# Performance work log

Hardware: AMD Instinct MI355X
Metric: run time of the kernel (lower is better)

The kernel has to match this reference:

```python
import jax, jax.numpy as jnp
import numpy as np

B, S, H = 64, 512, 768
N_SPANS, MAX_SPAN, CW = 4, 8, 3
NH = 8
HD = H // NH
W = MAX_SPAN + 1 + 2 * CW  # max context window length (15)
H2 = H // 2
N_ATE, N_SENT = 2, 2


def _ln(x, g, b, eps=1e-5):
    m = x.mean(-1, keepdims=True)
    v = ((x - m) ** 2).mean(-1, keepdims=True)
    return (x - m) / jnp.sqrt(v + eps) * g + b


def _classifier(x, w1, b1, g, bb, w2, b2):
    # Dropout -> Linear -> GELU -> LayerNorm -> Linear (eval mode: dropout = id)
    h = jax.nn.gelu(x @ w1.T + b1, approximate=False)
    h = _ln(h, g, bb)
    return h @ w2.T + b2


def setup_inputs() -> dict:
    key = jax.random.key(0)
    ks = jax.random.split(key, 16)
    p = lambda k, shape: (0.02 * jax.random.normal(k, shape)).astype(jnp.float32)
    seq_out = jax.random.normal(ks[0], (B, S, H), dtype=jnp.float32)
    starts = jax.random.randint(ks[1], (B, N_SPANS), 1, S - MAX_SPAN - 1)
    lens = jax.random.randint(ks[2], (B, N_SPANS), 1, MAX_SPAN + 1)
    ends = starts + lens  # exclusive end, span length in [1, MAX_SPAN]
    return dict(
        seq_out=seq_out,
        span_starts=starts.astype(jnp.int32),
        span_ends=ends.astype(jnp.int32),
        ate_g=jnp.ones((H,), jnp.float32), ate_b=jnp.zeros((H,), jnp.float32),
        apc_g=jnp.ones((H,), jnp.float32), apc_b=jnp.zeros((H,), jnp.float32),
        w_in=p(ks[3], (3 * H, H)), b_in=jnp.zeros((3 * H,), jnp.float32),
        w_out=p(ks[4], (H, H)), b_out=jnp.zeros((H,), jnp.float32),
        fus_w=p(ks[5], (H, 2 * H)), fus_b=jnp.zeros((H,), jnp.float32),
        asp_w1=p(ks[6], (H2, H)), asp_b1=jnp.zeros((H2,), jnp.float32),
        asp_lng=jnp.ones((H2,), jnp.float32), asp_lnb=jnp.zeros((H2,), jnp.float32),
        asp_w2=p(ks[7], (N_ATE, H2)), asp_b2=jnp.zeros((N_ATE,), jnp.float32),
        sen_w1=p(ks[8], (H2, H)), sen_b1=jnp.zeros((H2,), jnp.float32),
        sen_lng=jnp.ones((H2,), jnp.float32), sen_lnb=jnp.zeros((H2,), jnp.float32),
        sen_w2=p(ks[9], (N_SENT, H2)), sen_b2=jnp.zeros((N_SENT,), jnp.float32),
    )


def _fwd(seq_out, ate_g, ate_b, apc_g, apc_b, w_in, b_in, w_out, b_out,
         fus_w, fus_b, asp_w1, asp_b1, asp_lng, asp_lnb, asp_w2, asp_b2,
         sen_w1, sen_b1, sen_lng, sen_lnb, sen_w2, sen_b2,
         span_starts, span_ends):
    dt = seq_out.dtype
    # clamping semantics as in the torch loop
    s = jnp.clip(span_starts, 0, S - 1)
    e = jnp.maximum(s, jnp.minimum(span_ends, S - 1))
    left = jnp.maximum(0, s - CW)
    right = jnp.minimum(S, e + 1 + CW)

    # ATE head over all tokens
    ate_logits = _classifier(_ln(seq_out, ate_g, ate_b),
                             asp_w1, asp_b1, asp_lng, asp_lnb, asp_w2, asp_b2)

    gather = jax.vmap(lambda so, idx: so[idx])  # ([S,H],[N,W]) -> [N,W,H]

    # aspect mean over tokens [s, e)
    aidx = s[..., None] + jnp.arange(MAX_SPAN)          # [B,N,MS]
    va = (aidx < e[..., None]).astype(dt)
    asp_tok = gather(seq_out, jnp.clip(aidx, 0, S - 1)) # [B,N,MS,H]
    cnt = va.sum(-1, keepdims=True)                     # [B,N,1]
    asp_mean = (asp_tok * va[..., None]).sum(-2) / jnp.maximum(cnt, 1.0)
    asp_mean = jnp.where(cnt > 0, asp_mean, seq_out[:, None, 0, :])

    # context window [left, right): tiny self-attention, then mean
    cidx = left[..., None] + jnp.arange(W)              # [B,N,W]
    vc = (cidx < right[..., None]).astype(dt)
    ctx = gather(seq_out, jnp.clip(cidx, 0, S - 1))     # [B,N,W,H]
    qkv = ctx @ w_in.T + b_in
    q, k, v = jnp.split(qkv, 3, axis=-1)
    q = q.reshape(B, N_SPANS, W, NH, HD) * (HD ** -0.5)
    k = k.reshape(B, N_SPANS, W, NH, HD)
    v = v.reshape(B, N_SPANS, W, NH, HD)
    scores = jnp.einsum('bnqhd,bnkhd->bnhqk', q, k)
    neg = jnp.asarray(jnp.finfo(dt).min, dt)
    scores = jnp.where(vc[:, :, None, None, :] > 0, scores, neg)
    attn = jax.nn.softmax(scores, axis=-1)
    out = jnp.einsum('bnhqk,bnkhd->bnqhd', attn, v).reshape(B, N_SPANS, W, H)
    out = out @ w_out.T + b_out
    ccnt = vc.sum(-1, keepdims=True)
    ctx_mean = (out * vc[..., None]).sum(-2) / jnp.maximum(ccnt, 1.0)

    combined = jnp.concatenate([asp_mean, ctx_mean], axis=-1)  # [B,N,2H]
    fused = jax.nn.gelu(combined @ fus_w.T + fus_b, approximate=False)
    apc_feat = fused.mean(axis=1)                              # [B,H]
    apc_logits = _classifier(_ln(apc_feat, apc_g, apc_b),
                             sen_w1, sen_b1, sen_lng, sen_lnb, sen_w2, sen_b2)
    return ate_logits, apc_logits


def reference(seq_out, span_starts, span_ends, ate_g, ate_b, apc_g, apc_b,
              w_in, b_in, w_out, b_out, fus_w, fus_b,
              asp_w1, asp_b1, asp_lng, asp_lnb, asp_w2, asp_b2,
              sen_w1, sen_b1, sen_lng, sen_lnb, sen_w2, sen_b2):
    return _fwd(seq_out, ate_g, ate_b, apc_g, apc_b, w_in, b_in, w_out, b_out,
                fus_w, fus_b, asp_w1, asp_b1, asp_lng, asp_lnb, asp_w2, asp_b2,
                sen_w1, sen_b1, sen_lng, sen_lnb, sen_w2, sen_b2,
                span_starts, span_ends)
```

## Files before the change

### kernel.cpp

```cpp
#include <hip/hip_runtime.h>
#include <math.h>

#define DEVI __device__ __forceinline__

using bf16x8 = __attribute__((ext_vector_type(8))) short;
using f32x4  = __attribute__((ext_vector_type(4))) float;

DEVI float b2f(unsigned short u) {
  union { unsigned int u; float f; } x; x.u = ((unsigned int)u) << 16; return x.f;
}
DEVI unsigned short f2b(float f) {
  union { float f; unsigned int u; } x; x.f = f;
  unsigned int r = (x.u + 0x7fffu + ((x.u >> 16) & 1u)) >> 16;
  return (unsigned short)r;
}
DEVI float gelu_f(float x) { return 0.5f * x * (1.0f + erff(x * 0.70710678118654752440f)); }

DEVI void wredxor2(float& a, float& b) {
  #pragma unroll
  for (int off = 32; off; off >>= 1) {
    a += __shfl_xor(a, off);
    b += __shfl_xor(b, off);
  }
}

template<int NW>
DEVI void breduce2(float& a, float& b) {
  __shared__ float buf[2 * NW];
  int lane = threadIdx.x & 63;
  int w = threadIdx.x >> 6;
  #pragma unroll
  for (int off = 32; off > 0; off >>= 1) {
    a += __shfl_down(a, off);
    b += __shfl_down(b, off);
  }
  if (lane == 0) { buf[w] = a; buf[NW + w] = b; }
  __syncthreads();
  float ra = 0.f, rb = 0.f;
  #pragma unroll
  for (int i = 0; i < NW; ++i) { ra += buf[i]; rb += buf[NW + i]; }
  a = ra; b = rb;
  __syncthreads();
}

DEVI void span_params(const int* st, const int* en, int span,
                      int& s, int& e, int& left, int& right) {
  int s0 = st[span], e0 = en[span];
  s = min(max(s0, 0), 511);
  e = max(s, min(e0, 511));
  left = max(0, s - 3);
  right = min(512, e + 4);
}

DEVI int xcd_logical(int bid, int n) {
  int q = n >> 3, r = n & 7;
  int xcd = bid & 7, idx = bid >> 3;
  return (xcd < r ? xcd * (q + 1) : r * (q + 1) + (xcd - r) * q) + idx;
}

__global__ __launch_bounds__(256) void prep_kernel(
    const float* __restrict__ s0, const float* __restrict__ s1,
    const float* __restrict__ s2, const float* __restrict__ s3,
    const float* __restrict__ s4,
    unsigned short* __restrict__ d0, unsigned short* __restrict__ d1,
    unsigned short* __restrict__ d2, unsigned short* __restrict__ d3,
    unsigned short* __restrict__ d4,
    const float* __restrict__ seq, const float* __restrict__ ate_g,
    const float* __restrict__ ate_b, unsigned short* __restrict__ lnx,
    const int* __restrict__ st, const int* __restrict__ en,
    unsigned short* __restrict__ ctxA) {
  const int bid = blockIdx.x, tid = threadIdx.x;
  if (bid < 4032) {
    int i = bid * 256 + tid;
    const float* s; unsigned short* d; int j;
    if (i < 73728)       { s = s0; d = d0; j = i; }
    else if (i < 516096) { s = s1; d = d1; j = i - 73728; }
    else if (i < 663552) { s = s2; d = d2; j = i - 516096; }
    else if (i < 958464) { s = s3; d = d3; j = i - 663552; }
    else                 { s = s4; d = d4; j = i - 958464; }
    float4 v = reinterpret_cast<const float4*>(s)[j];
    ushort4 o;
    o.x = f2b(v.x); o.y = f2b(v.y); o.z = f2b(v.z); o.w = f2b(v.w);
    reinterpret_cast<ushort4*>(d)[j] = o;
  } else if (bid < 12224) {
    const int row = (bid - 4032) * 4 + (tid >> 6);
    const int lane = tid & 63;
    const float4* xr = reinterpret_cast<const float4*>(seq + (size_t)row * 768);
    float4 v[3];
    #pragma unroll
    for (int j = 0; j < 3; ++j) v[j] = xr[j * 64 + lane];
    float s = 0.f, q = 0.f;
    #pragma unroll
    for (int j = 0; j < 3; ++j) {
      s += v[j].x + v[j].y + v[j].z + v[j].w;
      q += v[j].x * v[j].x + v[j].y * v[j].y + v[j].z * v[j].z + v[j].w * v[j].w;
    }
    wredxor2(s, q);
    float mean = s * (1.0f / 768.0f);
    float rstd = rsqrtf(q * (1.0f / 768.0f) - mean * mean + 1e-5f);
    ushort4* orow = reinterpret_cast<ushort4*>(lnx + (size_t)row * 768);
    #pragma unroll
    for (int j = 0; j < 3; ++j) {
      float4 gv = reinterpret_cast<const float4*>(ate_g)[j * 64 + lane];
      float4 bv = reinterpret_cast<const float4*>(ate_b)[j * 64 + lane];
      ushort4 o;
      o.x = f2b((v[j].x - mean) * rstd * gv.x + bv.x);
      o.y = f2b((v[j].y - mean) * rstd * gv.y + bv.y);
      o.z = f2b((v[j].z - mean) * rstd * gv.z + bv.z);
      o.w = f2b((v[j].w - mean) * rstd * gv.w + bv.w);
      orow[j * 64 + lane] = o;
    }
  } else {
    if (tid >= 192) return;
    int r = bid - 12224;
    int span = r / 15, w = r % 15;
    int s, e, left, right;
    span_params(st, en, span, s, e, left, right);
    int b = span >> 2;
    int tok = min(left + w, 511);
    const float4* src = reinterpret_cast<const float4*>(seq + ((size_t)b * 512 + tok) * 768);
    ushort4* dst = reinterpret_cast<ushort4*>(ctxA + (size_t)r * 768);
    float4 v = src[tid];
    ushort4 o;
    o.x = f2b(v.x); o.y = f2b(v.y); o.z = f2b(v.z); o.w = f2b(v.w);
    dst[tid] = o;
  }
}

template<int BM, int BN, int WM, int WN>
DEVI void gemm_core(const unsigned short* __restrict__ A,
                    const unsigned short* __restrict__ W,
                    int K, int bm, int bn,
                    unsigned short* As, unsigned short* Bs,
                    f32x4 (&acc)[WM / 16][WN / 16]) {
  constexpr int CA = BM / 8;
  constexpr int CB = BN / 8;
  constexpr int NWC = BN / WN;
  constexpr int WAVES = (BM / WM) * NWC;
  constexpr int FM = WM / 16, FN = WN / 16;
  const int tid = threadIdx.x;
  const int lane = tid & 63;
  const int wv = tid >> 6;
  const int wr = wv / NWC, wc = wv % NWC;
  const int l16 = lane & 15, lhi = lane >> 4;
  const int srow = lane >> 3;
  const int scol = 8 * ((lane & 7) ^ srow);

  const int nt = K / 64;
  for (int t = 0; t < nt; ++t) {
    const int k0 = t * 64;
    #pragma unroll
    for (int ch = wv; ch < CA; ch += WAVES)
      __builtin_amdgcn_global_load_lds(
          (const __attribute__((address_space(1))) void*)&A[(size_t)(bm + ch * 8 + srow) * K + k0 + scol],
          (__attribute__((address_space(3))) void*)&As[ch * 512], 16, 0, 0);
    #pragma unroll
    for (int ch = wv; ch < CB; ch += WAVES)
      __builtin_amdgcn_global_load_lds(
          (const __attribute__((address_space(1))) void*)&W[(size_t)(bn + ch * 8 + srow) * K + k0 + scol],
          (__attribute__((address_space(3))) void*)&Bs[ch * 512], 16, 0, 0);
    __syncthreads();
    #pragma unroll
    for (int kk = 0; kk < 2; ++kk) {
      bf16x8 af[FM], bfr[FN];
      #pragma unroll
      for (int fm = 0; fm < FM; ++fm) {
        int r = wr * WM + fm * 16 + l16;
        af[fm] = *reinterpret_cast<const bf16x8*>(&As[r * 64 + ((kk * 32 + lhi * 8) ^ ((r & 7) * 8))]);
      }
      #pragma unroll
      for (int fn = 0; fn < FN; ++fn) {
        int r = wc * WN + fn * 16 + l16;
        bfr[fn] = *reinterpret_cast<const bf16x8*>(&Bs[r * 64 + ((kk * 32 + lhi * 8) ^ ((r & 7) * 8))]);
      }
      #pragma unroll
      for (int fm = 0; fm < FM; ++fm)
        #pragma unroll
        for (int fn = 0; fn < FN; ++fn)
          acc[fm][fn] = __builtin_amdgcn_mfma_f32_16x16x32_bf16(af[fm], bfr[fn], acc[fm][fn], 0, 0, 0);
    }
    __syncthreads();
  }
}

template<int BM, int BN, int WM, int WN>
DEVI void gemm_store(const float* __restrict__ bias, unsigned short* __restrict__ C,
                     int N, bool act, int bm, int bn, f32x4 (&acc)[WM / 16][WN / 16]) {
  constexpr int NWC = BN / WN;
  constexpr int FM = WM / 16, FN = WN / 16;
  const int lane = threadIdx.x & 63;
  const int wv = threadIdx.x >> 6;
  const int wr = wv / NWC, wc = wv % NWC;
  const int l16 = lane & 15, lhi = lane >> 4;
  #pragma unroll
  for (int fm = 0; fm < FM; ++fm) {
    #pragma unroll
    for (int fn = 0; fn < FN; ++fn) {
      int col = bn + wc * WN + fn * 16 + l16;
      float bv = bias[col];
      #pragma unroll
      for (int i = 0; i < 4; ++i) {
        int row = bm + wr * WM + fm * 16 + lhi * 4 + i;
        float v = acc[fm][fn][i] + bv;
        if (act) v = gelu_f(v);
        C[(size_t)row * N + col] = f2b(v);
      }
    }
  }
}

template<int BM, int BN, int WM, int WN, int ACT>
__global__ __launch_bounds__(256) void gemm_swz64(
    const unsigned short* __restrict__ A, const unsigned short* __restrict__ W,
    const float* __restrict__ bias, unsigned short* __restrict__ C,
    int M, int N, int K, int nbN) {
  __shared__ __align__(16) unsigned short As[BM * 64];
  __shared__ __align__(16) unsigned short Bs[BN * 64];
  int l = xcd_logical(blockIdx.x, gridDim.x);
  int mb = l / nbN, nb = l % nbN;
  f32x4 acc[WM / 16][WN / 16] = {};
  gemm_core<BM, BN, WM, WN>(A, W, K, mb * BM, nb * BN, As, Bs, acc);
  gemm_store<BM, BN, WM, WN>(bias, C, N, ACT != 0, mb * BM, nb * BN, acc);
}

__global__ __launch_bounds__(512) void dual_gemm_kernel(
    const unsigned short* __restrict__ lnx, const unsigned short* __restrict__ w1b,
    const float* __restrict__ b1, const float* __restrict__ lng,
    const float* __restrict__ w2, float4* __restrict__ hpart,
    const unsigned short* __restrict__ ctxA, const unsigned short* __restrict__ winb,
    const float* __restrict__ b_in, unsigned short* __restrict__ qkv) {
  __shared__ __align__(16) unsigned short lds[384 * 64];
  if (blockIdx.x < 384) {
    int l = xcd_logical(blockIdx.x, 384);
    int mb = l / 3, nb = l % 3;
    const int bm = mb * 256, bn = nb * 128;
    f32x4 acc[4][4] = {};
    gemm_core<256, 128, 64, 64>(lnx, w1b, 768, bm, bn, lds, lds + 256 * 64, acc);
    const int lane = threadIdx.x & 63;
    const int wv = threadIdx.x >> 6;
    const int wr = wv >> 1, wc = wv & 1;
    const int l16 = lane & 15, lhi = lane >> 4;
    float b1v[4], gw2a[4], gw2b[4];
    #pragma unroll
    for (int fn = 0; fn < 4; ++fn) {
      int col = bn + wc * 64 + fn * 16 + l16;
      b1v[fn] = b1[col];
      float gg = lng[col];
      gw2a[fn] = gg * w2[col];
      gw2b[fn] = gg * w2[384 + col];
    }
    #pragma unroll
    for (int fm = 0; fm < 4; ++fm) {
      #pragma unroll
      for (int i = 0; i < 4; ++i) {
        float s1 = 0.f, s2 = 0.f, q0 = 0.f, q1 = 0.f;
        #pragma unroll
        for (int fn = 0; fn < 4; ++fn) {
          float h = gelu_f(acc[fm][fn][i] + b1v[fn]);
          s1 += h; s2 += h * h;
          q0 += h * gw2a[fn]; q1 += h * gw2b[fn];
        }
        #pragma unroll
        for (int off = 1; off < 16; off <<= 1) {
          s1 += __shfl_xor(s1, off); s2 += __shfl_xor(s2, off);
          q0 += __shfl_xor(q0, off); q1 += __shfl_xor(q1, off);
        }
        if (l16 == 0) {
          int row = bm + wr * 64 + fm * 16 + lhi * 4 + i;
          hpart[(size_t)row * 6 + nb * 2 + wc] = make_float4(s1, s2, q0, q1);
        }
      }
    }
  } else {
    int bid = blockIdx.x - 384;
    int l = xcd_logical(bid, 270);
    int mb = l / 9, nb = l % 9;
    f32x4 acc[4][4] = {};
    gemm_core<128, 256, 64, 64>(ctxA, winb, 768, mb * 128, nb * 256,
                                lds, lds + 128 * 64, acc);
    gemm_store<128, 256, 64, 64>(b_in, qkv, 2304, false, mb * 128, nb * 256, acc);
  }
}

__global__ __launch_bounds__(256) void finattn_kernel(
    const float4* __restrict__ hpart, const float* __restrict__ lng,
    const float* __restrict__ lnb, const float* __restrict__ w2,
    const float* __restrict__ b2, float* __restrict__ out,
    const unsigned short* __restrict__ qkv, const int* __restrict__ st,
    const int* __restrict__ en, unsigned short* __restrict__ ctxO) {
  const int tid = threadIdx.x;
  if (blockIdx.x >= 2048) {
    __shared__ float cbuf[16];
    float c1a = 0.f, c1b = 0.f, c2a = 0.f, c2b = 0.f;
    for (int c = tid; c < 384; c += 256) {
      float gg = lng[c], bbv = lnb[c], wa = w2[c], wb = w2[384 + c];
      c1a += gg * wa; c1b += gg * wb;
      c2a += bbv * wa; c2b += bbv * wb;
    }
    wredxor2(c1a, c1b);
    wredxor2(c2a, c2b);
    if ((tid & 63) == 0) {
      int w = tid >> 6;
      cbuf[w * 4] = c1a; cbuf[w * 4 + 1] = c1b;
      cbuf[w * 4 + 2] = c2a; cbuf[w * 4 + 3] = c2b;
    }
    __syncthreads();
    c1a = cbuf[0] + cbuf[4] + cbuf[8] + cbuf[12];
    c1b = cbuf[1] + cbuf[5] + cbuf[9] + cbuf[13];
    c2a = cbuf[2] + cbuf[6] + cbuf[10] + cbuf[14];
    c2b = cbuf[3] + cbuf[7] + cbuf[11] + cbuf[15];
    const int row = (blockIdx.x - 2048) * 256 + tid;
    float S1 = 0.f, S2 = 0.f, D0 = 0.f, D1 = 0.f;
    #pragma unroll
    for (int p = 0; p < 6; ++p) {
      float4 v = hpart[(size_t)row * 6 + p];
      S1 += v.x; S2 += v.y; D0 += v.z; D1 += v.w;
    }
    float mu = S1 * (1.f / 384.f);
    float rstd = rsqrtf(S2 * (1.f / 384.f) - mu * mu + 1e-5f);
    out[(size_t)row * 2]     = rstd * (D0 - mu * c1a) + c2a + b2[0];
    out[(size_t)row * 2 + 1] = rstd * (D1 - mu * c1b) + c2b + b2[1];
    return;
  }
  __shared__ float qs[15][96], ks[15][96], vs[15][96];
  __shared__ float sc[15][16];
  const int span = blockIdx.x >> 3, hh = blockIdx.x & 7;
  int s, e, left, right;
  span_params(st, en, span, s, e, left, right);
  const int nv = right - left;
  const int r0 = span * 15;
  const float scale = 0.10206207261596576f;
  if (tid < 180) {
    int w = tid / 12, dp = tid % 12, d = dp * 8;
    const unsigned short* rowp = qkv + (size_t)(r0 + w) * 2304 + hh * 96 + d;
    bf16x8 qv = *reinterpret_cast<const bf16x8*>(rowp);
    bf16x8 kv = *reinterpret_cast<const bf16x8*>(rowp + 768);
    bf16x8 vv = *reinterpret_cast<const bf16x8*>(rowp + 1536);
    #pragma unroll
    for (int j = 0; j < 8; ++j) {
      qs[w][d + j] = b2f((unsigned short)qv[j]) * scale;
      ks[w][d + j] = b2f((unsigned short)kv[j]);
      vs[w][d + j] = b2f((unsigned short)vv[j]);
    }
  }
  __syncthreads();
  if (tid < 225) {
    int i = tid / 15, j = tid % 15;
    float a = 0.f;
    #pragma unroll
    for (int d = 0; d < 96; ++d) a += qs[i][d] * ks[j][d];
    sc[i][j] = (j < nv) ? a : -3.402823466e38f;
  }
  __syncthreads();
  if (tid < 15) {
    int i = tid;
    float m = -3.402823466e38f;
    #pragma unroll
    for (int j = 0; j < 15; ++j) m = fmaxf(m, sc[i][j]);
    float ex[15];
    float ssum = 0.f;
    #pragma unroll
    for (int j = 0; j < 15; ++j) { ex[j] = expf(sc[i][j] - m); ssum += ex[j]; }
    float inv = 1.0f / ssum;
    #pragma unroll
    for (int j = 0; j < 15; ++j) sc[i][j] = ex[j] * inv;
  }
  __syncthreads();
  for (int idx = tid; idx < 720; idx += 256) {
    int w = idx / 48, dp = idx % 48, d = dp * 2;
    float o0 = 0.f, o1 = 0.f;
    #pragma unroll
    for (int j = 0; j < 15; ++j) {
      float p = sc[w][j];
      o0 += p * vs[j][d];
      o1 += p * vs[j][d + 1];
    }
    ushort2 o; o.x = f2b(o0); o.y = f2b(o1);
    *reinterpret_cast<ushort2*>(&ctxO[(size_t)(r0 + w) * 768 + hh * 96 + d]) = o;
  }
}

__global__ __launch_bounds__(256) void means_kernel(
    const float* __restrict__ seq, const unsigned short* __restrict__ projO,
    const int* __restrict__ st, const int* __restrict__ en,
    unsigned short* __restrict__ comb) {
  const int span = blockIdx.x;
  int s, e, left, right;
  span_params(st, en, span, s, e, left, right);
  int b = span >> 2;
  int e2 = min(e, s + 8);
  int cnt = e2 - s;
  int nv = right - left;
  float inva = (cnt > 0) ? 1.0f / (float)cnt : 0.f;
  float invc = 1.0f / (float)nv;
  for (int c = threadIdx.x; c < 768; c += 256) {
    float sa = 0.f;
    for (int t = s; t < e2; ++t) sa += seq[((size_t)b * 512 + t) * 768 + c];
    float asp = (cnt > 0) ? sa * inva : seq[((size_t)b * 512) * 768 + c];
    comb[(size_t)span * 1536 + c] = f2b(asp);
    float sc_ = 0.f;
    for (int w = 0; w < nv; ++w) sc_ += b2f(projO[(size_t)(span * 15 + w) * 768 + c]);
    comb[(size_t)span * 1536 + 768 + c] = f2b(sc_ * invc);
  }
}

__global__ __launch_bounds__(256) void apc_all_kernel(
    const unsigned short* __restrict__ fused, const float* __restrict__ g,
    const float* __restrict__ bb, const unsigned short* __restrict__ senb,
    const float* __restrict__ b1, const float* __restrict__ lng,
    const float* __restrict__ lnb, const float* __restrict__ w2,
    const float* __restrict__ b2, float* __restrict__ out) {
  const int b = blockIdx.x, tid = threadIdx.x;
  __shared__ float xs[768];
  __shared__ float hs[384];
  float v[3];
  #pragma unroll
  for (int j = 0; j < 3; ++j) {
    int c = tid + j * 256;
    float a = 0.f;
    #pragma unroll
    for (int n = 0; n < 4; ++n) a += b2f(fused[((size_t)(b * 4 + n)) * 768 + c]);
    v[j] = 0.25f * a;
  }
  float s = v[0] + v[1] + v[2];
  float q = v[0] * v[0] + v[1] * v[1] + v[2] * v[2];
  breduce2<4>(s, q);
  float mean = s * (1.f / 768.f);
  float rstd = rsqrtf(q * (1.f / 768.f) - mean * mean + 1e-5f);
  #pragma unroll
  for (int j = 0; j < 3; ++j) {
    int c = tid + j * 256;
    xs[c] = (v[j] - mean) * rstd * g[c] + bb[c];
  }
  __syncthreads();
  for (int j = tid; j < 384; j += 256) {
    const bf16x8* wrp = reinterpret_cast<const bf16x8*>(senb + (size_t)j * 768);
    float dot = 0.f;
    #pragma unroll 4
    for (int k8 = 0; k8 < 96; ++k8) {
      bf16x8 wv = wrp[k8];
      #pragma unroll
      for (int u = 0; u < 8; ++u) dot += xs[k8 * 8 + u] * b2f((unsigned short)wv[u]);
    }
    hs[j] = gelu_f(dot + b1[j]);
  }
  __syncthreads();
  s = 0.f; q = 0.f;
  for (int j = tid; j < 384; j += 256) { float h = hs[j]; s += h; q += h * h; }
  breduce2<4>(s, q);
  mean = s * (1.f / 384.f);
  rstd = rsqrtf(q * (1.f / 384.f) - mean * mean + 1e-5f);
  float p0 = 0.f, p1 = 0.f;
  for (int j = tid; j < 384; j += 256) {
    float hl = (hs[j] - mean) * rstd * lng[j] + lnb[j];
    p0 += hl * w2[j];
    p1 += hl * w2[384 + j];
  }
  breduce2<4>(p0, p1);
  if (tid == 0) {
    out[b * 2]     = p0 + b2[0];
    out[b * 2 + 1] = p1 + b2[1];
  }
}

extern "C" void kernel_launch(void* const* d_in, const int* in_sizes, int n_in,
                              void* d_out, int out_size, void* d_ws, size_t ws_size,
                              hipStream_t stream) {
  const float* seq    = (const float*)d_in[0];
  const int*   st     = (const int*)d_in[1];
  const int*   en     = (const int*)d_in[2];
  const float* ate_g  = (const float*)d_in[3];
  const float* ate_b  = (const float*)d_in[4];
  const float* apc_g  = (const float*)d_in[5];
  const float* apc_b  = (const float*)d_in[6];
  const float* w_in   = (const float*)d_in[7];
  const float* b_in   = (const float*)d_in[8];
  const float* w_out  = (const float*)d_in[9];
  const float* b_out  = (const float*)d_in[10];
  const float* fus_w  = (const float*)d_in[11];
  const float* fus_b  = (const float*)d_in[12];
  const float* asp_w1 = (const float*)d_in[13];
  const float* asp_b1 = (const float*)d_in[14];
  const float* asp_lng= (const float*)d_in[15];
  const float* asp_lnb= (const float*)d_in[16];
  const float* asp_w2 = (const float*)d_in[17];
  const float* asp_b2 = (const float*)d_in[18];
  const float* sen_w1 = (const float*)d_in[19];
  const float* sen_b1 = (const float*)d_in[20];
  const float* sen_lng= (const float*)d_in[21];
  const float* sen_lnb= (const float*)d_in[22];
  const float* sen_w2 = (const float*)d_in[23];
  const float* sen_b2 = (const float*)d_in[24];
  float* out = (float*)d_out;

  char* wsb = (char*)d_ws;
  unsigned short* lnx   = (unsigned short*)(wsb + 0);
  unsigned short* ctxA  = (unsigned short*)(wsb + 52428800);
  unsigned short* qkvb  = (unsigned short*)(wsb + 58720256);
  unsigned short* ctxO  = (unsigned short*)(wsb + 77594624);
  unsigned short* projO = (unsigned short*)(wsb + 83886080);
  unsigned short* comb  = (unsigned short*)(wsb + 89849856);
  unsigned short* fusO  = (unsigned short*)(wsb + 90636288);
  const size_t off_w = 91275264;
  float4*        hpart  = (float4*)(wsb + off_w);
  const size_t off_w2 = off_w + 25165824;
  unsigned short* w1b   = (unsigned short*)(wsb + off_w2);
  unsigned short* winb  = (unsigned short*)(wsb + off_w2 + 589824);
  unsigned short* woutb = (unsigned short*)(wsb + off_w2 + 4128768);
  unsigned short* fusb  = (unsigned short*)(wsb + off_w2 + 5308416);
  unsigned short* senb  = (unsigned short*)(wsb + off_w2 + 7667712);

  prep_kernel<<<16064, 256, 0, stream>>>(asp_w1, w_in, w_out, fus_w, sen_w1,
                                         w1b, winb, woutb, fusb, senb,
                                         seq, ate_g, ate_b, lnx, st, en, ctxA);
  dual_gemm_kernel<<<654, 512, 0, stream>>>(lnx, w1b, asp_b1, asp_lng, asp_w2, hpart,
                                            ctxA, winb, b_in, qkvb);
  finattn_kernel<<<2176, 256, 0, stream>>>(hpart, asp_lng, asp_lnb, asp_w2, asp_b2, out,
                                           qkvb, st, en, ctxO);
  gemm_swz64<64, 128, 32, 64, 0><<<360, 256, 0, stream>>>(
      ctxO, woutb, b_out, projO, 3840, 768, 768, 6);
  means_kernel<<<256, 256, 0, stream>>>(seq, projO, st, en, comb);
  gemm_swz64<64, 64, 32, 32, 1><<<48, 256, 0, stream>>>(
      comb, fusb, fus_b, fusO, 256, 768, 1536, 12);
  apc_all_kernel<<<64, 256, 0, stream>>>(fusO, apc_g, apc_b, senb, sen_b1,
                                         sen_lng, sen_lnb, sen_w2, sen_b2, out + 65536);
}
```

Before: 183.2 us.

## Fold LayerNorm into ATE GEMM epilogue and gather context rows via token map

The ATE LayerNorm is now applied algebraically. The gamma scale is folded into the bf16 W1 weights, and per-row (rstd, rstd*mean) stats plus per-column gamma·W and beta·W sums correct the raw-input GEMM in the epilogue. As a result one bf16 copy of seq serves the ATE GEMM, the QKV GEMM (through a row index map instead of a materialized context copy) and the means kernel, which now reads bf16 instead of fp32. This cuts the separate normalized-activation and context buffers and the related traffic. In exchange it adds a tiny serial dot-product pass for the correction sums, and the algebraic LN in bf16 carries some precision risk.

```diff
diff --git a/kernel.cpp b/kernel.cpp
--- a/kernel.cpp
+++ b/kernel.cpp
@@ -59,25 +59,35 @@
 }
 
 __global__ __launch_bounds__(256) void prep_kernel(
-    const float* __restrict__ s0, const float* __restrict__ s1,
-    const float* __restrict__ s2, const float* __restrict__ s3,
-    const float* __restrict__ s4,
+    const float* __restrict__ w1, const float* __restrict__ w_in,
+    const float* __restrict__ w_out, const float* __restrict__ fus_w,
+    const float* __restrict__ sen_w1,
     unsigned short* __restrict__ d0, unsigned short* __restrict__ d1,
     unsigned short* __restrict__ d2, unsigned short* __restrict__ d3,
     unsigned short* __restrict__ d4,
     const float* __restrict__ seq, const float* __restrict__ ate_g,
-    const float* __restrict__ ate_b, unsigned short* __restrict__ lnx,
+    const float* __restrict__ ate_b, unsigned short* __restrict__ sbf,
+    float2* __restrict__ stats, float2* __restrict__ c12,
     const int* __restrict__ st, const int* __restrict__ en,
-    unsigned short* __restrict__ ctxA) {
+    int* __restrict__ tokmap) {
   const int bid = blockIdx.x, tid = threadIdx.x;
   if (bid < 4032) {
     int i = bid * 256 + tid;
+    if (i < 73728) {
+      float4 v = reinterpret_cast<const float4*>(w1)[i];
+      int k0 = (i * 4) % 768;
+      float4 gv = *reinterpret_cast<const float4*>(ate_g + k0);
+      ushort4 o;
+      o.x = f2b(v.x * gv.x); o.y = f2b(v.y * gv.y);
+      o.z = f2b(v.z * gv.z); o.w = f2b(v.w * gv.w);
+      reinterpret_cast<ushort4*>(d0)[i] = o;
+      return;
+    }
     const float* s; unsigned short* d; int j;
-    if (i < 73728)       { s = s0; d = d0; j = i; }
-    else if (i < 516096) { s = s1; d = d1; j = i - 73728; }
-    else if (i < 663552) { s = s2; d = d2; j = i - 516096; }
-    else if (i < 958464) { s = s3; d = d3; j = i - 663552; }
-    else                 { s = s4; d = d4; j = i - 958464; }
+    if (i < 516096)      { s = w_in;   d = d1; j = i - 73728; }
+    else if (i < 663552) { s = w_out;  d = d2; j = i - 516096; }
+    else if (i < 958464) { s = fus_w;  d = d3; j = i - 663552; }
+    else                 { s = sen_w1; d = d4; j = i - 958464; }
     float4 v = reinterpret_cast<const float4*>(s)[j];
     ushort4 o;
     o.x = f2b(v.x); o.y = f2b(v.y); o.z = f2b(v.z); o.w = f2b(v.w);
@@ -98,32 +108,34 @@
     wredxor2(s, q);
     float mean = s * (1.0f / 768.0f);
     float rstd = rsqrtf(q * (1.0f / 768.0f) - mean * mean + 1e-5f);
-    ushort4* orow = reinterpret_cast<ushort4*>(lnx + (size_t)row * 768);
+    ushort4* orow = reinterpret_cast<ushort4*>(sbf + (size_t)row * 768);
     #pragma unroll
     for (int j = 0; j < 3; ++j) {
-      float4 gv = reinterpret_cast<const float4*>(ate_g)[j * 64 + lane];
-      float4 bv = reinterpret_cast<const float4*>(ate_b)[j * 64 + lane];
       ushort4 o;
-      o.x = f2b((v[j].x - mean) * rstd * gv.x + bv.x);
-      o.y = f2b((v[j].y - mean) * rstd * gv.y + bv.y);
-      o.z = f2b((v[j].z - mean) * rstd * gv.z + bv.z);
-      o.w = f2b((v[j].w - mean) * rstd * gv.w + bv.w);
+      o.x = f2b(v[j].x); o.y = f2b(v[j].y); o.z = f2b(v[j].z); o.w = f2b(v[j].w);
       orow[j * 64 + lane] = o;
     }
+    if (lane == 0) stats[row] = make_float2(rstd, rstd * mean);
+  } else if (bid < 12226) {
+    int j = (bid - 12224) * 256 + tid;
+    if (j < 384) {
+      const float* wr = w1 + (size_t)j * 768;
+      float a = 0.f, bsum = 0.f;
+      for (int k = 0; k < 768; ++k) {
+        float wv = wr[k];
+        a += ate_g[k] * wv;
+        bsum += ate_b[k] * wv;
+      }
+      c12[j] = make_float2(a, bsum);
+    }
   } else {
-    if (tid >= 192) return;
-    int r = bid - 12224;
-    int span = r / 15, w = r % 15;
-    int s, e, left, right;
-    span_params(st, en, span, s, e, left, right);
-    int b = span >> 2;
-    int tok = min(left + w, 511);
-    const float4* src = reinterpret_cast<const float4*>(seq + ((size_t)b * 512 + tok) * 768);
-    ushort4* dst = reinterpret_cast<ushort4*>(ctxA + (size_t)r * 768);
-    float4 v = src[tid];
-    ushort4 o;
-    o.x = f2b(v.x); o.y = f2b(v.y); o.z = f2b(v.z); o.w = f2b(v.w);
-    dst[tid] = o;
+    for (int i = tid; i < 3840; i += 256) {
+      int span = i / 15, w = i % 15;
+      int s, e, left, right;
+      span_params(st, en, span, s, e, left, right);
+      int b = span >> 2;
+      tokmap[i] = b * 512 + min(left + w, 511);
+    }
   }
 }
 
@@ -132,7 +144,8 @@
                     const unsigned short* __restrict__ W,
                     int K, int bm, int bn,
                     unsigned short* As, unsigned short* Bs,
-                    f32x4 (&acc)[WM / 16][WN / 16]) {
+                    f32x4 (&acc)[WM / 16][WN / 16],
+                    const int* __restrict__ rowmap = nullptr) {
   constexpr int CA = BM / 8;
   constexpr int CB = BN / 8;
   constexpr int NWC = BN / WN;
@@ -150,10 +163,13 @@
   for (int t = 0; t < nt; ++t) {
     const int k0 = t * 64;
     #pragma unroll
-    for (int ch = wv; ch < CA; ch += WAVES)
+    for (int ch = wv; ch < CA; ch += WAVES) {
+      int ar = bm + ch * 8 + srow;
+      size_t arow = rowmap ? (size_t)rowmap[ar] : (size_t)ar;
       __builtin_amdgcn_global_load_lds(
-          (const __attribute__((address_space(1))) void*)&A[(size_t)(bm + ch * 8 + srow) * K + k0 + scol],
+          (const __attribute__((address_space(1))) void*)&A[arow * K + k0 + scol],
           (__attribute__((address_space(3))) void*)&As[ch * 512], 16, 0, 0);
+    }
     #pragma unroll
     for (int ch = wv; ch < CB; ch += WAVES)
       __builtin_amdgcn_global_load_lds(
@@ -224,27 +240,30 @@
 }
 
 __global__ __launch_bounds__(512) void dual_gemm_kernel(
-    const unsigned short* __restrict__ lnx, const unsigned short* __restrict__ w1b,
-    const float* __restrict__ b1, const float* __restrict__ lng,
+    const unsigned short* __restrict__ sbf, const unsigned short* __restrict__ w1b,
+    const float* __restrict__ b1, const float2* __restrict__ c12,
+    const float2* __restrict__ stats, const float* __restrict__ lng,
     const float* __restrict__ w2, float4* __restrict__ hpart,
-    const unsigned short* __restrict__ ctxA, const unsigned short* __restrict__ winb,
-    const float* __restrict__ b_in, unsigned short* __restrict__ qkv) {
+    const unsigned short* __restrict__ winb, const float* __restrict__ b_in,
+    unsigned short* __restrict__ qkv, const int* __restrict__ tokmap) {
   __shared__ __align__(16) unsigned short lds[384 * 64];
   if (blockIdx.x < 384) {
     int l = xcd_logical(blockIdx.x, 384);
     int mb = l / 3, nb = l % 3;
     const int bm = mb * 256, bn = nb * 128;
     f32x4 acc[4][4] = {};
-    gemm_core<256, 128, 64, 64>(lnx, w1b, 768, bm, bn, lds, lds + 256 * 64, acc);
+    gemm_core<256, 128, 64, 64>(sbf, w1b, 768, bm, bn, lds, lds + 256 * 64, acc);
     const int lane = threadIdx.x & 63;
     const int wv = threadIdx.x >> 6;
     const int wr = wv >> 1, wc = wv & 1;
     const int l16 = lane & 15, lhi = lane >> 4;
-    float b1v[4], gw2a[4], gw2b[4];
+    float b1v[4], gw2a[4], gw2b[4], c1v[4], c2v[4];
     #pragma unroll
     for (int fn = 0; fn < 4; ++fn) {
       int col = bn + wc * 64 + fn * 16 + l16;
       b1v[fn] = b1[col];
+      float2 cc = c12[col];
+      c1v[fn] = cc.x; c2v[fn] = cc.y;
       float gg = lng[col];
       gw2a[fn] = gg * w2[col];
       gw2b[fn] = gg * w2[384 + col];
@@ -253,10 +272,12 @@
     for (int fm = 0; fm < 4; ++fm) {
       #pragma unroll
       for (int i = 0; i < 4; ++i) {
+        int row = bm + wr * 64 + fm * 16 + lhi * 4 + i;
+        float2 sr = stats[row];
         float s1 = 0.f, s2 = 0.f, q0 = 0.f, q1 = 0.f;
         #pragma unroll
         for (int fn = 0; fn < 4; ++fn) {
-          float h = gelu_f(acc[fm][fn][i] + b1v[fn]);
+          float h = gelu_f(sr.x * acc[fm][fn][i] - sr.y * c1v[fn] + c2v[fn] + b1v[fn]);
           s1 += h; s2 += h * h;
           q0 += h * gw2a[fn]; q1 += h * gw2b[fn];
         }
@@ -265,10 +286,7 @@
           s1 += __shfl_xor(s1, off); s2 += __shfl_xor(s2, off);
           q0 += __shfl_xor(q0, off); q1 += __shfl_xor(q1, off);
         }
-        if (l16 == 0) {
-          int row = bm + wr * 64 + fm * 16 + lhi * 4 + i;
-          hpart[(size_t)row * 6 + nb * 2 + wc] = make_float4(s1, s2, q0, q1);
-        }
+        if (l16 == 0) hpart[(size_t)row * 6 + nb * 2 + wc] = make_float4(s1, s2, q0, q1);
       }
     }
   } else {
@@ -276,8 +294,8 @@
     int l = xcd_logical(bid, 270);
     int mb = l / 9, nb = l % 9;
     f32x4 acc[4][4] = {};
-    gemm_core<128, 256, 64, 64>(ctxA, winb, 768, mb * 128, nb * 256,
-                                lds, lds + 128 * 64, acc);
+    gemm_core<128, 256, 64, 64>(sbf, winb, 768, mb * 128, nb * 256,
+                                lds, lds + 128 * 64, acc, tokmap);
     gemm_store<128, 256, 64, 64>(b_in, qkv, 2304, false, mb * 128, nb * 256, acc);
   }
 }
@@ -381,7 +399,7 @@
 }
 
 __global__ __launch_bounds__(256) void means_kernel(
-    const float* __restrict__ seq, const unsigned short* __restrict__ projO,
+    const unsigned short* __restrict__ sbf, const unsigned short* __restrict__ projO,
     const int* __restrict__ st, const int* __restrict__ en,
     unsigned short* __restrict__ comb) {
   const int span = blockIdx.x;
@@ -395,8 +413,8 @@
   float invc = 1.0f / (float)nv;
   for (int c = threadIdx.x; c < 768; c += 256) {
     float sa = 0.f;
-    for (int t = s; t < e2; ++t) sa += seq[((size_t)b * 512 + t) * 768 + c];
-    float asp = (cnt > 0) ? sa * inva : seq[((size_t)b * 512) * 768 + c];
+    for (int t = s; t < e2; ++t) sa += b2f(sbf[((size_t)b * 512 + t) * 768 + c]);
+    float asp = (cnt > 0) ? sa * inva : b2f(sbf[((size_t)b * 512) * 768 + c]);
     comb[(size_t)span * 1536 + c] = f2b(asp);
     float sc_ = 0.f;
     for (int w = 0; w < nv; ++w) sc_ += b2f(projO[(size_t)(span * 15 + w) * 768 + c]);
@@ -494,32 +512,35 @@
   float* out = (float*)d_out;
 
   char* wsb = (char*)d_ws;
-  unsigned short* lnx   = (unsigned short*)(wsb + 0);
-  unsigned short* ctxA  = (unsigned short*)(wsb + 52428800);
-  unsigned short* qkvb  = (unsigned short*)(wsb + 58720256);
-  unsigned short* ctxO  = (unsigned short*)(wsb + 77594624);
-  unsigned short* projO = (unsigned short*)(wsb + 83886080);
-  unsigned short* comb  = (unsigned short*)(wsb + 89849856);
-  unsigned short* fusO  = (unsigned short*)(wsb + 90636288);
-  const size_t off_w = 91275264;
-  float4*        hpart  = (float4*)(wsb + off_w);
-  const size_t off_w2 = off_w + 25165824;
-  unsigned short* w1b   = (unsigned short*)(wsb + off_w2);
-  unsigned short* winb  = (unsigned short*)(wsb + off_w2 + 589824);
-  unsigned short* woutb = (unsigned short*)(wsb + off_w2 + 4128768);
-  unsigned short* fusb  = (unsigned short*)(wsb + off_w2 + 5308416);
-  unsigned short* senb  = (unsigned short*)(wsb + off_w2 + 7667712);
-
-  prep_kernel<<<16064, 256, 0, stream>>>(asp_w1, w_in, w_out, fus_w, sen_w1,
+  unsigned short* sbf   = (unsigned short*)(wsb + 0);
+  float2*        stats  = (float2*)(wsb + 50331648);
+  float2*        c12    = (float2*)(wsb + 50593792);
+  int*           tokmap = (int*)(wsb + 50596864);
+  unsigned short* qkvb  = (unsigned short*)(wsb + 50612224);
+  unsigned short* ctxO  = (unsigned short*)(wsb + 68306944);
+  unsigned short* projO = (unsigned short*)(wsb + 74205184);
+  unsigned short* comb  = (unsigned short*)(wsb + 80103424);
+  unsigned short* fusO  = (unsigned short*)(wsb + 80889856);
+  float4*        hpart  = (float4*)(wsb + 81283072);
+  const size_t off_w = 84428800;
+  unsigned short* w1b   = (unsigned short*)(wsb + off_w);
+  unsigned short* winb  = (unsigned short*)(wsb + off_w + 589824);
+  unsigned short* woutb = (unsigned short*)(wsb + off_w + 4128768);
+  unsigned short* fusb  = (unsigned short*)(wsb + off_w + 5308416);
+  unsigned short* senb  = (unsigned short*)(wsb + off_w + 7667712);
+
+  prep_kernel<<<12227, 256, 0, stream>>>(asp_w1, w_in, w_out, fus_w, sen_w1,
                                          w1b, winb, woutb, fusb, senb,
-                                         seq, ate_g, ate_b, lnx, st, en, ctxA);
-  dual_gemm_kernel<<<654, 512, 0, stream>>>(lnx, w1b, asp_b1, asp_lng, asp_w2, hpart,
-                                            ctxA, winb, b_in, qkvb);
+                                         seq, ate_g, ate_b, sbf, stats, c12,
+                                         st, en, tokmap);
+  dual_gemm_kernel<<<654, 512, 0, stream>>>(sbf, w1b, asp_b1, c12, stats,
+                                            asp_lng, asp_w2, hpart,
+                                            winb, b_in, qkvb, tokmap);
   finattn_kernel<<<2176, 256, 0, stream>>>(hpart, asp_lng, asp_lnb, asp_w2, asp_b2, out,
                                            qkvb, st, en, ctxO);
   gemm_swz64<64, 128, 32, 64, 0><<<360, 256, 0, stream>>>(
       ctxO, woutb, b_out, projO, 3840, 768, 768, 6);
-  means_kernel<<<256, 256, 0, stream>>>(seq, projO, st, en, comb);
+  means_kernel<<<256, 256, 0, stream>>>(sbf, projO, st, en, comb);
   gemm_swz64<64, 64, 32, 32, 1><<<48, 256, 0, stream>>>(
       comb, fusb, fus_b, fusO, 256, 768, 1536, 12);
   apc_all_kernel<<<64, 256, 0, stream>>>(fusO, apc_g, apc_b, senb, sen_b1,
```

After: 204.9 us. 11.8% more time.
